# Optimization experiments

Measured on AMD Instinct MI355X. Metric: run time of the kernel, lower is better.

The kernel has to match this reference:

```python
import jax, jax.numpy as jnp
import numpy as np

C, G, NH, NE = 640, 32, 8, 512
B, H, W, P = 8, 32, 32, 77
HD = C // NH
EPS = 1e-5


def _groupnorm(x, g, b):
    # x: (B, C, H, W); normalize over (C//G, H, W) within each of G groups
    bb, cc, hh, ww = x.shape
    xg = x.reshape(bb, G, cc // G, hh, ww)
    mu = xg.mean(axis=(2, 3, 4), keepdims=True)
    var = xg.var(axis=(2, 3, 4), keepdims=True)
    xg = (xg - mu) * jax.lax.rsqrt(var + EPS)
    return xg.reshape(bb, cc, hh, ww) * g[None, :, None, None] + b[None, :, None, None]


def _layernorm(x, g, b):
    mu = x.mean(axis=-1, keepdims=True)
    var = x.var(axis=-1, keepdims=True)
    return (x - mu) * jax.lax.rsqrt(var + EPS) * g + b


def _split_heads(t):
    # (B, S, C) -> (B, NH, S, HD)
    bb, ss, _ = t.shape
    return t.reshape(bb, ss, NH, HD).transpose(0, 2, 1, 3)


def _attn(q, k, v):
    # q,k,v: (B, NH, S, HD) — manual softmax(q k^T / sqrt(d)) v, as in the source
    scores = jnp.einsum('bhqd,bhkd->bhqk', q, k) / (HD ** 0.5)
    probs = jax.nn.softmax(scores, axis=-1)
    out = jnp.einsum('bhqk,bhkd->bhqd', probs, v)
    bb = q.shape[0]
    return out.transpose(0, 2, 1, 3).reshape(bb, q.shape[2], C)


def unet_attention_fwd(x, p, gn_g, gn_b, ci_w, ci_b, ln1_g, ln1_b,
                       qkv_w, qkv_b, saw_w, saw_b, ln2_g, ln2_b,
                       caq_w, caq_b, cak_w, cak_b, cav_w, cav_b, caw_w, caw_b,
                       ln3_g, ln3_b, g1_w, g1_b, g2_w, g2_b, co_w, co_b):
    residue_long = x
    h = _groupnorm(x, gn_g, gn_b)
    # conv_input: 1x1 conv == per-pixel linear; ci_w: (C_in, C_out)
    h = jnp.einsum('bihw,io->bohw', h, ci_w) + ci_b[None, :, None, None]
    bb, cc, hh, ww = h.shape
    h = h.reshape(bb, cc, hh * ww).transpose(0, 2, 1)  # (B, HW, C)

    # self attention
    res = h
    t = _layernorm(h, ln1_g, ln1_b)
    qkv = t @ qkv_w + qkv_b
    q, k, v = jnp.split(qkv, 3, axis=-1)
    t = _attn(_split_heads(q), _split_heads(k), _split_heads(v))
    h = res + (t @ saw_w + saw_b)

    # cross attention (prompt p: (B, 77, NE))
    res = h
    t = _layernorm(h, ln2_g, ln2_b)
    q = t @ caq_w + caq_b
    k = p @ cak_w + cak_b
    v = p @ cav_w + cav_b
    t = _attn(_split_heads(q), _split_heads(k), _split_heads(v))
    h = res + (t @ caw_w + caw_b)

    # GEGLU MLP (exact GELU, matching torch F.gelu default)
    res = h
    t = _layernorm(h, ln3_g, ln3_b)
    proj = t @ g1_w + g1_b  # (B, HW, 8C)
    a, gate = jnp.split(proj, 2, axis=-1)
    t = a * jax.nn.gelu(gate, approximate=False)
    h = res + (t @ g2_w + g2_b)

    h = h.transpose(0, 2, 1).reshape(bb, cc, hh, ww)
    out = jnp.einsum('bihw,io->bohw', h, co_w) + co_b[None, :, None, None]
    return out + residue_long


def setup_inputs() -> dict:
    keys = jax.random.split(jax.random.key(0), 20)
    ki = iter(keys)
    s = 0.02

    def w(shape):
        return jax.random.normal(next(ki), shape, jnp.float32) * s

    return {
        'x': jax.random.normal(next(ki), (B, C, H, W), jnp.float32),
        'p': jax.random.normal(next(ki), (B, P, NE), jnp.float32),
        'gn_g': jnp.ones((C,), jnp.float32), 'gn_b': jnp.zeros((C,), jnp.float32),
        'ci_w': w((C, C)), 'ci_b': jnp.zeros((C,), jnp.float32),
        'ln1_g': jnp.ones((C,), jnp.float32), 'ln1_b': jnp.zeros((C,), jnp.float32),
        'qkv_w': w((C, 3 * C)), 'qkv_b': jnp.zeros((3 * C,), jnp.float32),
        'saw_w': w((C, C)), 'saw_b': jnp.zeros((C,), jnp.float32),
        'ln2_g': jnp.ones((C,), jnp.float32), 'ln2_b': jnp.zeros((C,), jnp.float32),
        'caq_w': w((C, C)), 'caq_b': jnp.zeros((C,), jnp.float32),
        'cak_w': w((NE, C)), 'cak_b': jnp.zeros((C,), jnp.float32),
        'cav_w': w((NE, C)), 'cav_b': jnp.zeros((C,), jnp.float32),
        'caw_w': w((C, C)), 'caw_b': jnp.zeros((C,), jnp.float32),
        'ln3_g': jnp.ones((C,), jnp.float32), 'ln3_b': jnp.zeros((C,), jnp.float32),
        'g1_w': w((C, 8 * C)), 'g1_b': jnp.zeros((8 * C,), jnp.float32),
        'g2_w': w((4 * C, C)), 'g2_b': jnp.zeros((C,), jnp.float32),
        'co_w': w((C, C)), 'co_b': jnp.zeros((C,), jnp.float32),
    }


def reference(x, p, gn_g, gn_b, ci_w, ci_b, ln1_g, ln1_b,
              qkv_w, qkv_b, saw_w, saw_b, ln2_g, ln2_b,
              caq_w, caq_b, cak_w, cak_b, cav_w, cav_b, caw_w, caw_b,
              ln3_g, ln3_b, g1_w, g1_b, g2_w, g2_b, co_w, co_b):
    return unet_attention_fwd(x, p, gn_g, gn_b, ci_w, ci_b, ln1_g, ln1_b,
                              qkv_w, qkv_b, saw_w, saw_b, ln2_g, ln2_b,
                              caq_w, caq_b, cak_w, cak_b, cav_w, cav_b, caw_w, caw_b,
                              ln3_g, ln3_b, g1_w, g1_b, g2_w, g2_b, co_w, co_b)
```

## Files before the change

### kernel.cpp

```cpp
#include <hip/hip_runtime.h>
#include <math.h>

typedef unsigned short u16;
typedef __attribute__((ext_vector_type(8))) short short8;
typedef __attribute__((ext_vector_type(4))) float f32x4;

#define DI static __device__ __forceinline__

DI float bf2f(u16 u) { union { unsigned u; float f; } c; c.u = (unsigned)u << 16; return c.f; }
DI u16 f2bf(float f) {
  union { float f; unsigned u; } c; c.f = f;
  unsigned r = c.u + 0x7fffu + ((c.u >> 16) & 1u);
  return (u16)(r >> 16);
}

DI void gload16(const u16* g, u16* l) {
  __builtin_amdgcn_global_load_lds(
      (const __attribute__((address_space(1))) unsigned int*)g,
      (__attribute__((address_space(3))) unsigned int*)l, 16, 0, 0);
}

DI void xcd_swz(int& bx, int& by, int gx, int gy) {
  int id = by * gx + bx;
  int n = gx * gy;
  int q = n >> 3, r = n & 7;
  int xcd = id & 7, k = id >> 3;
  int s = (xcd < r) ? (xcd * (q + 1) + k) : (r * (q + 1) + (xcd - r) * q + k);
  bx = s % gx;
  by = s / gx;
}

struct PrepDesc { const float* src; u16* dst; int K, N, nbx, boff, perm; };
struct PrepArgs { PrepDesc d[10]; };

__global__ __launch_bounds__(256) void prep_all(PrepArgs a) {
  int bid = blockIdx.x;
  int i = 0;
  while (i < 9 && bid >= a.d[i + 1].boff) i++;
  const PrepDesc D = a.d[i];
  int rel = bid - D.boff;
  int bx = rel % D.nbx, by = rel / D.nbx;
  int K = D.K, N = D.N;
  __shared__ float tile[32][33];
  int k0 = by * 32, n0 = bx * 32;
  int tid = threadIdx.x;
  int ni = tid & 31, ki8 = tid >> 5;
  for (int q = 0; q < 4; q++) {
    int k = ki8 + q * 8;
    tile[k][ni] = D.src[(size_t)(k0 + k) * N + n0 + ni];
  }
  __syncthreads();
  int kj = tid & 31, nj8 = tid >> 5;
  for (int q = 0; q < 4; q++) {
    int n = nj8 + q * 8;
    int nold = n0 + n;
    int rowp = nold;
    if (D.perm) {
      rowp = (nold < 2560) ? ((nold >> 5) * 64 + (nold & 31))
                           : (((nold - 2560) >> 5) * 64 + 32 + (nold & 31));
    }
    D.dst[(size_t)rowp * K + k0 + kj] = f2bf(tile[kj][n]);
  }
}

__global__ __launch_bounds__(256) void conv_bf16(const float* __restrict__ in,
                                                 u16* __restrict__ out, long n) {
  long i = (long)blockIdx.x * 256 + threadIdx.x;
  if (i < n) out[i] = f2bf(in[i]);
}

__global__ __launch_bounds__(256) void concat2(const float* __restrict__ a,
                                               const float* __restrict__ b,
                                               float* __restrict__ o, int n) {
  int i = blockIdx.x * 256 + threadIdx.x;
  if (i < n) o[i] = a[i];
  else if (i < 2 * n) o[i] = b[i - n];
}

__global__ __launch_bounds__(256) void gn_stats(const float* __restrict__ x,
                                                float* __restrict__ mean_o,
                                                float* __restrict__ rstd_o) {
  int bg = blockIdx.x;
  const float4* p = (const float4*)(x + (size_t)bg * 20480);
  float s = 0.f, sq = 0.f;
  for (int i = threadIdx.x; i < 5120; i += 256) {
    float4 v = p[i];
    s += v.x + v.y + v.z + v.w;
    sq += v.x * v.x + v.y * v.y + v.z * v.z + v.w * v.w;
  }
  for (int off = 1; off < 64; off <<= 1) { s += __shfl_xor(s, off); sq += __shfl_xor(sq, off); }
  __shared__ float ps[4], pq[4];
  int w = threadIdx.x >> 6;
  if ((threadIdx.x & 63) == 0) { ps[w] = s; pq[w] = sq; }
  __syncthreads();
  if (threadIdx.x == 0) {
    float S = ps[0] + ps[1] + ps[2] + ps[3];
    float Q = pq[0] + pq[1] + pq[2] + pq[3];
    float mu = S / 20480.f;
    float var = Q / 20480.f - mu * mu;
    mean_o[bg] = mu;
    rstd_o[bg] = rsqrtf(var + 1e-5f);
  }
}

__global__ __launch_bounds__(256) void gn_apply(const float* __restrict__ x,
                                                const float* __restrict__ mean_,
                                                const float* __restrict__ rstd_,
                                                const float* __restrict__ g,
                                                const float* __restrict__ bb,
                                                u16* __restrict__ out) {
  __shared__ float tile[32][33];
  int b = blockIdx.z, c0 = blockIdx.y * 32, s0 = blockIdx.x * 32;
  int tid = threadIdx.x;
  int si = tid & 31, ci8 = tid >> 5;
  for (int i = 0; i < 4; i++) {
    int c = c0 + ci8 + i * 8;
    int gg = c / 20;
    float mu = mean_[b * 32 + gg], rs = rstd_[b * 32 + gg];
    float v = x[((size_t)b * 640 + c) * 1024 + s0 + si];
    tile[ci8 + i * 8][si] = (v - mu) * rs * g[c] + bb[c];
  }
  __syncthreads();
  int cj = tid & 31, sj8 = tid >> 5;
  for (int i = 0; i < 4; i++) {
    int sj = sj8 + i * 8;
    out[((size_t)b * 1024 + s0 + sj) * 640 + c0 + cj] = f2bf(tile[cj][sj]);
  }
}

__global__ __launch_bounds__(256) void ln_kernel(const float* __restrict__ in,
                                                 const float* __restrict__ g,
                                                 const float* __restrict__ bb,
                                                 u16* __restrict__ out) {
  int t = blockIdx.x * 4 + (threadIdx.x >> 6);
  int lane = threadIdx.x & 63;
  const float* row = in + (size_t)t * 640;
  float xv[10], s = 0.f, sq = 0.f;
  for (int j = 0; j < 10; j++) {
    xv[j] = row[lane + j * 64];
    s += xv[j];
    sq += xv[j] * xv[j];
  }
  for (int off = 1; off < 64; off <<= 1) { s += __shfl_xor(s, off); sq += __shfl_xor(sq, off); }
  float mu = s * (1.f / 640.f);
  float var = sq * (1.f / 640.f) - mu * mu;
  float rstd = rsqrtf(var + 1e-5f);
  for (int j = 0; j < 10; j++) {
    int c = lane + j * 64;
    out[(size_t)t * 640 + c] = f2bf((xv[j] - mu) * rstd * g[c] + bb[c]);
  }
}


DI const short8* fragp(const u16* unit, int row, int g4) {
  int off = row * 64 + g4 * 16;
  off ^= ((off >> 7) & 3) << 4;
  return (const short8*)((const char*)unit + off);
}

template <int MODE>
__global__ __launch_bounds__(512, 1) void gemm256(const u16* __restrict__ A,
                                                  const u16* __restrict__ Bt,
                                                  const float* __restrict__ bias,
                                                  void* outp, const float* res,
                                                  int M, int N, int K) {
  __shared__ __align__(16) u16 As[4][8192];
  __shared__ __align__(16) u16 Bs[4][8192];
  const int tid = threadIdx.x;
  const int lane = tid & 63, wid = tid >> 6;
  const int wm = wid >> 2, wn = wid & 3;
  const int rq = lane & 15, g4 = lane >> 4;
  int bx = blockIdx.x, by = blockIdx.y;
  xcd_swz(bx, by, gridDim.x, gridDim.y);
  const int m0 = bx * 256, n0 = by * 256;

  int D0 = tid * 16;
  int so = D0 ^ (((D0 >> 7) & 3) << 4);
  const int srow = so >> 6;
  const int sk16 = (so & 63) >> 1;

  f32x4 acc[8][4] = {};
  const int nt = K >> 5;

#define STG_A(kt)                                                              \
  {                                                                            \
    gload16(A + (size_t)(m0 + srow) * K + (kt)*32 + sk16,                      \
            &As[(kt) & 3][0] + tid * 8);                                       \
    gload16(A + (size_t)(m0 + 128 + srow) * K + (kt)*32 + sk16,                \
            &As[(kt) & 3][4096] + tid * 8);                                    \
  }
#define STG_B(kt)                                                              \
  {                                                                            \
    gload16(Bt + (size_t)(n0 + srow) * K + (kt)*32 + sk16,                     \
            &Bs[(kt) & 3][0] + tid * 8);                                       \
    gload16(Bt + (size_t)(n0 + 128 + srow) * K + (kt)*32 + sk16,               \
            &Bs[(kt) & 3][4096] + tid * 8);                                    \
  }
#define BAR asm volatile("s_barrier" ::: "memory")

#define PH1(T)                                                                 \
  {                                                                            \
    const u16* Au = &As[(T) & 3][0];                                           \
    const u16* Bu = &Bs[(T) & 3][0];                                           \
    _Pragma("unroll") for (int i = 0; i < 4; i++)                              \
        af[i] = *fragp(Au, wm * 128 + i * 16 + rq, g4);                        \
    _Pragma("unroll") for (int j = 0; j < 4; j++)                              \
        bf[j] = *fragp(Bu, wn * 64 + j * 16 + rq, g4);                         \
    BAR;                                                                       \
    asm volatile("s_waitcnt lgkmcnt(0)" ::: "memory");                         \
    __builtin_amdgcn_sched_barrier(0);                                         \
    __builtin_amdgcn_s_setprio(1);                                             \
    _Pragma("unroll") for (int i = 0; i < 4; i++)                              \
        _Pragma("unroll") for (int j = 0; j < 4; j++)                          \
            acc[i][j] =                                                        \
        __builtin_amdgcn_mfma_f32_16x16x32_bf16(af[i], bf[j], acc[i][j], 0, 0, 0); \
    __builtin_amdgcn_s_setprio(0);                                             \
  }

#define PH2(T, DO_STG, WSTR)                                                   \
  {                                                                            \
    const u16* Au = &As[(T) & 3][0];                                           \
    _Pragma("unroll") for (int i = 0; i < 4; i++)                              \
        af[i] = *fragp(Au, wm * 128 + 64 + i * 16 + rq, g4);                   \
    if (DO_STG) { STG_A((T) + 3); STG_B((T) + 3); }                            \
    asm volatile(WSTR ::: "memory");                                           \
    BAR;                                                                       \
    asm volatile("s_waitcnt lgkmcnt(0)" ::: "memory");                         \
    __builtin_amdgcn_sched_barrier(0);                                         \
    __builtin_amdgcn_s_setprio(1);                                             \
    _Pragma("unroll") for (int i = 0; i < 4; i++)                              \
        _Pragma("unroll") for (int j = 0; j < 4; j++)                          \
            acc[4 + i][j] =                                                    \
        __builtin_amdgcn_mfma_f32_16x16x32_bf16(af[i], bf[j], acc[4 + i][j], 0, 0, 0); \
    __builtin_amdgcn_s_setprio(0);                                             \
  }

  STG_A(0); STG_B(0); STG_A(1); STG_B(1); STG_A(2); STG_B(2);
  asm volatile("s_waitcnt vmcnt(8)" ::: "memory");
  BAR;

  short8 af[4], bf[4];
  int t = 0;
  for (; t < nt - 3; t++) {
    PH1(t);
    PH2(t, true, "s_waitcnt vmcnt(8)");
  }
  PH1(t); PH2(t, false, "s_waitcnt vmcnt(4)"); t++;
  PH1(t); PH2(t, false, "s_waitcnt vmcnt(0)"); t++;
  PH1(t); PH2(t, false, "s_nop 0");

  if (MODE == 5) {
#pragma unroll
    for (int mf = 0; mf < 8; mf++) {
      int mb = m0 + wm * 128 + mf * 16 + g4 * 4;
#pragma unroll
      for (int j = 0; j < 2; j++) {
        int n = n0 + wn * 64 + j * 16 + rq;
        int c = (n >> 6) * 32 + (n & 31);
        float ba = bias[c];
        float bg = bias[2560 + c];
#pragma unroll
        for (int r = 0; r < 4; r++) {
          float a = acc[mf][j][r] + ba;
          float gt = acc[mf][j + 2][r] + bg;
          float gl = 0.5f * gt * (1.f + erff(gt * 0.70710678f));
          ((u16*)outp)[(size_t)(mb + r) * 2560 + c] = f2bf(a * gl);
        }
      }
    }
  } else {
#pragma unroll
    for (int mf = 0; mf < 8; mf++) {
#pragma unroll
      for (int j = 0; j < 4; j++) {
        int n = n0 + wn * 64 + j * 16 + rq;
        if (n >= N) continue;
        float bv = bias[n];
        int mb = m0 + wm * 128 + mf * 16 + g4 * 4;
        f32x4 v = acc[mf][j];
#pragma unroll
        for (int r = 0; r < 4; r++) {
          size_t o = (size_t)(mb + r) * N + n;
          ((u16*)outp)[o] = f2bf(v[r] + bv);
        }
      }
    }
  }
  (void)res;
#undef STG_A
#undef STG_B
#undef PH1
#undef PH2
#undef BAR
}

template <int MODE>
__global__ __launch_bounds__(256) void gemm_bt(const u16* __restrict__ A,
                                               const u16* __restrict__ Bt,
                                               const float* __restrict__ bias,
                                               void* outp, const float* res,
                                               int M, int N, int K) {
  __shared__ __align__(16) u16 As[4][128 * 32];
  __shared__ __align__(16) u16 Bs[4][128 * 32];
  const int tid = threadIdx.x;
  const int lane = tid & 63, wid = tid >> 6;
  const int wm = wid >> 1, wn = wid & 1;
  int bx = blockIdx.x, by = blockIdx.y;
  xcd_swz(bx, by, gridDim.x, gridDim.y);
  const int m0 = bx * 128, n0 = by * 128;
  const int rq = lane & 15, g4 = lane >> 4;

  const int srow = tid >> 2;
  const int scol = tid & 3;
  int gmA0 = m0 + srow;        if (gmA0 >= M) gmA0 = M - 1;
  int gmA1 = m0 + 64 + srow;   if (gmA1 >= M) gmA1 = M - 1;
  const u16* gA0 = A + (size_t)gmA0 * K + scol * 8;
  const u16* gA1 = A + (size_t)gmA1 * K + scol * 8;
  const u16* gB0 = Bt + (size_t)(n0 + srow) * K + scol * 8;
  const u16* gB1 = Bt + (size_t)(n0 + 64 + srow) * K + scol * 8;
  u16* lA0 = &As[0][srow * 32 + scol * 8];
  u16* lA1 = &As[0][(64 + srow) * 32 + scol * 8];
  u16* lB0 = &Bs[0][srow * 32 + scol * 8];
  u16* lB1 = &Bs[0][(64 + srow) * 32 + scol * 8];

  f32x4 acc[4][4] = {};

  auto STAGE = [&](int buf, int k0) {
    int o = buf * (128 * 32);
    gload16(gA0 + k0, lA0 + o);
    gload16(gA1 + k0, lA1 + o);
    gload16(gB0 + k0, lB0 + o);
    gload16(gB1 + k0, lB1 + o);
  };
  auto COMPUTE = [&](int buf) {
    short8 af[4], bfr[4];
    for (int i = 0; i < 4; i++)
      af[i] = *(const short8*)&As[buf][(wm * 64 + i * 16 + rq) * 32 + g4 * 8];
    for (int j = 0; j < 4; j++)
      bfr[j] = *(const short8*)&Bs[buf][(wn * 64 + j * 16 + rq) * 32 + g4 * 8];
    __builtin_amdgcn_s_setprio(1);
    for (int i = 0; i < 4; i++)
      for (int j = 0; j < 4; j++)
        acc[i][j] = __builtin_amdgcn_mfma_f32_16x16x32_bf16(af[i], bfr[j], acc[i][j], 0, 0, 0);
    __builtin_amdgcn_s_setprio(0);
  };

  const int nk = K >> 5;
  STAGE(0, 0);
  STAGE(1, 32);
  int t = 0;
  for (; t < nk - 2; t++) {
    STAGE((t + 2) & 3, (t + 2) << 5);
    asm volatile("s_waitcnt vmcnt(8)" ::: "memory");
    __builtin_amdgcn_s_barrier();
    COMPUTE(t & 3);
  }
  asm volatile("s_waitcnt vmcnt(4)" ::: "memory");
  __builtin_amdgcn_s_barrier();
  COMPUTE(t & 3);
  t++;
  asm volatile("s_waitcnt vmcnt(0)" ::: "memory");
  __builtin_amdgcn_s_barrier();
  COMPUTE(t & 3);

  for (int j = 0; j < 4; j++) {
    int n = n0 + wn * 64 + j * 16 + rq;
    float bv = bias[n];
    for (int i = 0; i < 4; i++) {
      int mb = m0 + wm * 64 + i * 16 + g4 * 4;
      f32x4 v = acc[i][j];
      if (MODE == 3) {
        int b = mb >> 10, sp = mb & 1023;
        size_t o = ((size_t)b * 640 + n) * 1024 + sp;
        f32x4 xv = *(const f32x4*)(res + o);
        f32x4 ov;
        for (int r = 0; r < 4; r++) ov[r] = v[r] + bv + xv[r];
        *(f32x4*)((float*)outp + o) = ov;
      } else {
        for (int r = 0; r < 4; r++) {
          int m = mb + r;
          if (m >= M) break;
          size_t o = (size_t)m * N + n;
          float val = v[r] + bv;
          if (MODE == 0)
            ((float*)outp)[o] = val;
          else if (MODE == 1)
            ((u16*)outp)[o] = f2bf(val);
          else if (MODE == 2)
            ((float*)outp)[o] = val + res[o];
          else
            ((u16*)outp)[o] = f2bf(val + res[o]);
        }
      }
    }
  }
}

__global__ __launch_bounds__(256) void attn_kernel(const u16* __restrict__ Qb, int ldq, long qbs,
                                                   const u16* __restrict__ Kb, int ldk, long kbs,
                                                   const u16* __restrict__ Vb,
                                                   u16* __restrict__ Ob, int ldo, long obs,
                                                   int Sk, float scale) {
  __shared__ __align__(16) u16 Ks[64 * 96];
  __shared__ __align__(16) u16 Vt[80 * 64];
  __shared__ __align__(16) u16 Ps[4][16 * 72];
  const short8 zero = {0, 0, 0, 0, 0, 0, 0, 0};
  const int tid = threadIdx.x;
  const int lane = tid & 63, w = tid >> 6;
  const int rq = lane & 15, g4 = lane >> 4;
  const int b = blockIdx.z, h = blockIdx.y;
  const u16* Q = Qb + (size_t)b * qbs + h * 80;
  const u16* Kp = Kb + (size_t)b * kbs + h * 80;
  const u16* Vp = Vb + (size_t)b * kbs + h * 80;
  u16* Op = Ob + (size_t)b * obs + h * 80;
  const int q0 = blockIdx.x * 64 + w * 16;
  const float Af = scale * 1.44269504f;

  short8 qa[3];
#pragma unroll
  for (int kk = 0; kk < 3; kk++) {
    int d = kk * 32 + g4 * 8;
    qa[kk] = (d < 80) ? *(const short8*)(Q + (size_t)(q0 + rq) * ldq + d) : zero;
  }
  f32x4 oacc[5] = {};
  float m_run = -1e30f, l_run = 0.f;

  const int nkt = (Sk + 63) >> 6;
  for (int kt = 0; kt < nkt; kt++) {
    const int kbase = kt * 64;
    for (int s = tid; s < 768; s += 256) {
      int row = s / 12, c = s % 12;
      int kidx = kbase + row;
      short8 v = zero;
      if (c < 10 && kidx < Sk) v = *(const short8*)(Kp + (size_t)kidx * ldk + c * 8);
      int byte = row * 192 + c * 16;
      byte ^= (row & 7) << 4;
      *(short8*)((char*)Ks + byte) = v;
    }
    for (int s = tid; s < 320; s += 256) {
      int k2 = (s & 31) * 2, c = s >> 5;
      int k0i = kbase + k2;
      short8 v0 = zero, v1 = zero;
      if (k0i < Sk) v0 = *(const short8*)(Vp + (size_t)k0i * ldk + c * 8);
      if (k0i + 1 < Sk) v1 = *(const short8*)(Vp + (size_t)(k0i + 1) * ldk + c * 8);
#pragma unroll
      for (int jj = 0; jj < 8; jj++) {
        int d = c * 8 + jj;
        unsigned cm = (unsigned)(u16)v0[jj] | ((unsigned)(u16)v1[jj] << 16);
        int byte = d * 128 + k2 * 2;
        byte ^= (d & 7) << 4;
        *(unsigned*)((char*)Vt + byte) = cm;
      }
    }
    __syncthreads();

    f32x4 sc[4] = {};
#pragma unroll
    for (int n = 0; n < 4; n++)
#pragma unroll
      for (int kk = 0; kk < 3; kk++) {
        int row = n * 16 + rq;
        int byte = row * 192 + (kk * 32 + g4 * 8) * 2;
        byte ^= (rq & 7) << 4;
        short8 kb = *(const short8*)((const char*)Ks + byte);
        sc[n] = __builtin_amdgcn_mfma_f32_16x16x32_bf16(kb, qa[kk], sc[n], 0, 0, 0);
      }
    const bool full = (kbase + 64 <= Sk);
    if (!full) {
#pragma unroll
      for (int n = 0; n < 4; n++)
#pragma unroll
        for (int r = 0; r < 4; r++)
          if (kbase + n * 16 + g4 * 4 + r >= Sk) sc[n][r] = -1e30f;
    }
    float t0 = fmaxf(fmaxf(sc[0][0], sc[0][1]), fmaxf(sc[0][2], sc[0][3]));
    float t1 = fmaxf(fmaxf(sc[1][0], sc[1][1]), fmaxf(sc[1][2], sc[1][3]));
    float t2 = fmaxf(fmaxf(sc[2][0], sc[2][1]), fmaxf(sc[2][2], sc[2][3]));
    float t3 = fmaxf(fmaxf(sc[3][0], sc[3][1]), fmaxf(sc[3][2], sc[3][3]));
    float tm = fmaxf(fmaxf(t0, t1), fmaxf(t2, t3));
    tm = fmaxf(tm, __shfl_xor(tm, 16));
    tm = fmaxf(tm, __shfl_xor(tm, 32));
    if (!__all(tm <= m_run + 48.0f)) {
      float mn = fmaxf(m_run, tm);
      float sf = exp2f(Af * (m_run - mn));
      m_run = mn;
      l_run *= sf;
      float sfo[4];
#pragma unroll
      for (int r = 0; r < 4; r++) sfo[r] = __shfl(sf, g4 * 4 + r);
#pragma unroll
      for (int nn = 0; nn < 5; nn++)
#pragma unroll
        for (int r = 0; r < 4; r++) oacc[nn][r] *= sfo[r];
    }
    const float Am = Af * m_run;
    float rs0 = 0.f, rs1 = 0.f;
#pragma unroll
    for (int n = 0; n < 4; n++) {
      float p0 = exp2f(fmaf(Af, sc[n][0], -Am));
      float p1 = exp2f(fmaf(Af, sc[n][1], -Am));
      float p2 = exp2f(fmaf(Af, sc[n][2], -Am));
      float p3 = exp2f(fmaf(Af, sc[n][3], -Am));
      sc[n][0] = p0; sc[n][1] = p1; sc[n][2] = p2; sc[n][3] = p3;
      rs0 += p0 + p1;
      rs1 += p2 + p3;
    }
    float rsum = rs0 + rs1;
    rsum += __shfl_xor(rsum, 16);
    rsum += __shfl_xor(rsum, 32);
    l_run += rsum;
#pragma unroll
    for (int n = 0; n < 4; n++) {
      unsigned pk0, pk1;
      asm("v_cvt_pk_bf16_f32 %0, %1, %2" : "=v"(pk0) : "v"(sc[n][0]), "v"(sc[n][1]));
      asm("v_cvt_pk_bf16_f32 %0, %1, %2" : "=v"(pk1) : "v"(sc[n][2]), "v"(sc[n][3]));
      int base = rq * 72 + n * 16 + g4 * 4;
      *(unsigned*)&Ps[w][base] = pk0;
      *(unsigned*)&Ps[w][base + 2] = pk1;
    }
    __builtin_amdgcn_s_setprio(1);
#pragma unroll
    for (int s = 0; s < 2; s++) {
      short8 pa = *(const short8*)&Ps[w][rq * 72 + s * 32 + g4 * 8];
#pragma unroll
      for (int nn = 0; nn < 5; nn++) {
        int row = nn * 16 + rq;
        int byte = row * 128 + (s * 32 + g4 * 8) * 2;
        byte ^= (rq & 7) << 4;
        short8 vb = *(const short8*)((const char*)Vt + byte);
        oacc[nn] = __builtin_amdgcn_mfma_f32_16x16x32_bf16(pa, vb, oacc[nn], 0, 0, 0);
      }
    }
    __builtin_amdgcn_s_setprio(0);
    __syncthreads();
  }
  float lo[4];
#pragma unroll
  for (int r = 0; r < 4; r++) lo[r] = 1.0f / __shfl(l_run, g4 * 4 + r);
#pragma unroll
  for (int nn = 0; nn < 5; nn++)
#pragma unroll
    for (int r = 0; r < 4; r++)
      Op[(size_t)(q0 + g4 * 4 + r) * ldo + nn * 16 + rq] = f2bf(oacc[nn][r] * lo[r]);
}

extern "C" void kernel_launch(void* const* d_in, const int* in_sizes, int n_in,
                              void* d_out, int out_size, void* d_ws, size_t ws_size,
                              hipStream_t stream) {
  (void)in_sizes; (void)n_in; (void)out_size; (void)ws_size;
  const float* x = (const float*)d_in[0];
  const float* p = (const float*)d_in[1];
  const float* gn_g = (const float*)d_in[2];
  const float* gn_b = (const float*)d_in[3];
  const float* ci_w = (const float*)d_in[4];
  const float* ci_b = (const float*)d_in[5];
  const float* ln1_g = (const float*)d_in[6];
  const float* ln1_b = (const float*)d_in[7];
  const float* qkv_w = (const float*)d_in[8];
  const float* qkv_b = (const float*)d_in[9];
  const float* saw_w = (const float*)d_in[10];
  const float* saw_b = (const float*)d_in[11];
  const float* ln2_g = (const float*)d_in[12];
  const float* ln2_b = (const float*)d_in[13];
  const float* caq_w = (const float*)d_in[14];
  const float* caq_b = (const float*)d_in[15];
  const float* cak_w = (const float*)d_in[16];
  const float* cak_b = (const float*)d_in[17];
  const float* cav_w = (const float*)d_in[18];
  const float* cav_b = (const float*)d_in[19];
  const float* caw_w = (const float*)d_in[20];
  const float* caw_b = (const float*)d_in[21];
  const float* ln3_g = (const float*)d_in[22];
  const float* ln3_b = (const float*)d_in[23];
  const float* g1_w = (const float*)d_in[24];
  const float* g1_b = (const float*)d_in[25];
  const float* g2_w = (const float*)d_in[26];
  const float* g2_b = (const float*)d_in[27];
  const float* co_w = (const float*)d_in[28];
  const float* co_b = (const float*)d_in[29];
  float* out = (float*)d_out;

  char* ws = (char*)d_ws;
  size_t off = 0;
  auto alloc = [&](size_t bytes) {
    size_t o = off;
    off += (bytes + 255) & ~(size_t)255;
    return o;
  };
  u16* WCI = (u16*)(ws + alloc((size_t)768 * 640 * 2));
  u16* WQKV = (u16*)(ws + alloc((size_t)2048 * 640 * 2));
  u16* WSAW = (u16*)(ws + alloc((size_t)768 * 640 * 2));
  u16* WCAQ = (u16*)(ws + alloc((size_t)768 * 640 * 2));
  u16* WCAKV = (u16*)(ws + alloc((size_t)1280 * 512 * 2));
  u16* WCAW = (u16*)(ws + alloc((size_t)768 * 640 * 2));
  u16* WG1 = (u16*)(ws + alloc((size_t)5120 * 640 * 2));
  u16* WG2 = (u16*)(ws + alloc((size_t)768 * 2560 * 2));
  u16* WCO = (u16*)(ws + alloc((size_t)768 * 640 * 2));
  u16* X = (u16*)(ws + alloc((size_t)8192 * 640 * 2));
  u16* Y = (u16*)(ws + alloc((size_t)8192 * 640 * 2));
  float* F1 = (float*)(ws + alloc((size_t)8192 * 640 * 4));
  u16* QKV = (u16*)(ws + alloc((size_t)8192 * 1920 * 2));
  u16* PBF = (u16*)(ws + alloc((size_t)616 * 512 * 2));
  u16* KVC = (u16*)(ws + alloc((size_t)616 * 1280 * 2));
  u16* TG = (u16*)(ws + alloc((size_t)8192 * 2560 * 2));
  float* GNM = (float*)(ws + alloc(256 * 4));
  float* GNR = (float*)(ws + alloc(256 * 4));
  float* CBIAS = (float*)(ws + alloc(1280 * 4));

  PrepArgs pa;
  int boff = 0;
  auto addw = [&](int idx, const float* src, u16* dst, int K, int N, int perm) {
    pa.d[idx].src = src; pa.d[idx].dst = dst;
    pa.d[idx].K = K; pa.d[idx].N = N;
    pa.d[idx].nbx = N / 32; pa.d[idx].boff = boff; pa.d[idx].perm = perm;
    boff += (N / 32) * (K / 32);
  };
  addw(0, ci_w, WCI, 640, 640, 0);
  addw(1, qkv_w, WQKV, 640, 1920, 0);
  addw(2, saw_w, WSAW, 640, 640, 0);
  addw(3, caq_w, WCAQ, 640, 640, 0);
  addw(4, cak_w, WCAKV, 512, 640, 0);
  addw(5, cav_w, WCAKV + (size_t)640 * 512, 512, 640, 0);
  addw(6, caw_w, WCAW, 640, 640, 0);
  addw(7, g1_w, WG1, 640, 5120, 1);
  addw(8, g2_w, WG2, 2560, 640, 0);
  addw(9, co_w, WCO, 640, 640, 0);
  prep_all<<<boff, 256, 0, stream>>>(pa);
  conv_bf16<<<1232, 256, 0, stream>>>(p, PBF, (long)616 * 512);
  concat2<<<5, 256, 0, stream>>>(cak_b, cav_b, CBIAS, 640);

  gn_stats<<<256, 256, 0, stream>>>(x, GNM, GNR);
  gn_apply<<<dim3(32, 20, 8), 256, 0, stream>>>(x, GNM, GNR, gn_g, gn_b, X);

  const float scale = 0.11180339887498949f;

  gemm_bt<0><<<dim3(64, 5), 256, 0, stream>>>(X, WCI, ci_b, F1, nullptr, 8192, 640, 640);
  ln_kernel<<<2048, 256, 0, stream>>>(F1, ln1_g, ln1_b, Y);
  gemm256<1><<<dim3(32, 8), 512, 0, stream>>>(Y, WQKV, qkv_b, QKV, nullptr, 8192, 1920, 640);
  attn_kernel<<<dim3(16, 8, 8), 256, 0, stream>>>(QKV, 1920, (long)1024 * 1920,
                                                  QKV + 640, 1920, (long)1024 * 1920,
                                                  QKV + 1280, X, 640, (long)1024 * 640,
                                                  1024, scale);
  gemm_bt<2><<<dim3(64, 5), 256, 0, stream>>>(X, WSAW, saw_b, F1, F1, 8192, 640, 640);
  ln_kernel<<<2048, 256, 0, stream>>>(F1, ln2_g, ln2_b, Y);
  gemm_bt<1><<<dim3(64, 5), 256, 0, stream>>>(Y, WCAQ, caq_b, X, nullptr, 8192, 640, 640);
  gemm_bt<1><<<dim3(5, 10), 256, 0, stream>>>(PBF, WCAKV, CBIAS, KVC, nullptr, 616, 1280, 512);
  attn_kernel<<<dim3(16, 8, 8), 256, 0, stream>>>(X, 640, (long)1024 * 640,
                                                  KVC, 1280, (long)77 * 1280,
                                                  KVC + 640, Y, 640, (long)1024 * 640,
                                                  77, scale);
  gemm_bt<2><<<dim3(64, 5), 256, 0, stream>>>(Y, WCAW, caw_b, F1, F1, 8192, 640, 640);
  ln_kernel<<<2048, 256, 0, stream>>>(F1, ln3_g, ln3_b, X);
  gemm256<5><<<dim3(32, 20), 512, 0, stream>>>(X, WG1, g1_b, TG, nullptr, 8192, 5120, 640);
  gemm_bt<4><<<dim3(64, 5), 256, 0, stream>>>(TG, WG2, g2_b, X, F1, 8192, 640, 2560);
  gemm_bt<3><<<dim3(64, 5), 256, 0, stream>>>(X, WCO, co_b, out, x, 8192, 640, 640);
}
```

Measured before the change: 475.2 us.

## Replace 256x256 GEMM with swizzled 128-tile and new 64x128 tile kernels

Removes the 512-thread 256x256 gemm256 kernel and routes the QKV and GEGLU GEMMs through the 128x128 gemm_bt, which gains a fused GEGLU epilogue. Adds a gemm_bt64 kernel with 64x128 tiles for all N=640 GEMMs, doubling the number of workgroups so the 256 CUs are better filled. Also switches gemm_bt's LDS layout to the XOR-swizzled fragment addressing to cut bank conflicts. In exchange, the smaller tiles give less operand reuse per block and use a simpler pipeline than the removed kernel.

New measurement: 486.4 us. 2.3% more time.

```diff
diff --git a/kernel.cpp b/kernel.cpp
--- a/kernel.cpp
+++ b/kernel.cpp
@@ -28,6 +28,12 @@
   int s = (xcd < r) ? (xcd * (q + 1) + k) : (r * (q + 1) + (xcd - r) * q + k);
   bx = s % gx;
   by = s / gx;
+}
+
+DI const short8* fragp(const u16* unit, int row, int g4) {
+  int off = row * 64 + g4 * 16;
+  off ^= ((off >> 7) & 3) << 4;
+  return (const short8*)((const char*)unit + off);
 }
 
 struct PrepDesc { const float* src; u16* dst; int K, N, nbx, boff, perm; };
@@ -151,147 +157,16 @@
   }
 }
 
-
-DI const short8* fragp(const u16* unit, int row, int g4) {
-  int off = row * 64 + g4 * 16;
-  off ^= ((off >> 7) & 3) << 4;
-  return (const short8*)((const char*)unit + off);
-}
-
 template <int MODE>
-__global__ __launch_bounds__(512, 1) void gemm256(const u16* __restrict__ A,
-                                                  const u16* __restrict__ Bt,
-                                                  const float* __restrict__ bias,
-                                                  void* outp, const float* res,
-                                                  int M, int N, int K) {
-  __shared__ __align__(16) u16 As[4][8192];
-  __shared__ __align__(16) u16 Bs[4][8192];
-  const int tid = threadIdx.x;
-  const int lane = tid & 63, wid = tid >> 6;
-  const int wm = wid >> 2, wn = wid & 3;
-  const int rq = lane & 15, g4 = lane >> 4;
-  int bx = blockIdx.x, by = blockIdx.y;
-  xcd_swz(bx, by, gridDim.x, gridDim.y);
-  const int m0 = bx * 256, n0 = by * 256;
-
-  int D0 = tid * 16;
-  int so = D0 ^ (((D0 >> 7) & 3) << 4);
-  const int srow = so >> 6;
-  const int sk16 = (so & 63) >> 1;
-
-  f32x4 acc[8][4] = {};
-  const int nt = K >> 5;
-
-#define STG_A(kt)                                                              \
-  {                                                                            \
-    gload16(A + (size_t)(m0 + srow) * K + (kt)*32 + sk16,                      \
-            &As[(kt) & 3][0] + tid * 8);                                       \
-    gload16(A + (size_t)(m0 + 128 + srow) * K + (kt)*32 + sk16,                \
-            &As[(kt) & 3][4096] + tid * 8);                                    \
-  }
-#define STG_B(kt)                                                              \
-  {                                                                            \
-    gload16(Bt + (size_t)(n0 + srow) * K + (kt)*32 + sk16,                     \
-            &Bs[(kt) & 3][0] + tid * 8);                                       \
-    gload16(Bt + (size_t)(n0 + 128 + srow) * K + (kt)*32 + sk16,               \
-            &Bs[(kt) & 3][4096] + tid * 8);                                    \
-  }
-#define BAR asm volatile("s_barrier" ::: "memory")
-
-#define PH1(T)                                                                 \
-  {                                                                            \
-    const u16* Au = &As[(T) & 3][0];                                           \
-    const u16* Bu = &Bs[(T) & 3][0];                                           \
-    _Pragma("unroll") for (int i = 0; i < 4; i++)                              \
-        af[i] = *fragp(Au, wm * 128 + i * 16 + rq, g4);                        \
-    _Pragma("unroll") for (int j = 0; j < 4; j++)                              \
-        bf[j] = *fragp(Bu, wn * 64 + j * 16 + rq, g4);                         \
-    BAR;                                                                       \
-    asm volatile("s_waitcnt lgkmcnt(0)" ::: "memory");                         \
-    __builtin_amdgcn_sched_barrier(0);                                         \
-    __builtin_amdgcn_s_setprio(1);                                             \
-    _Pragma("unroll") for (int i = 0; i < 4; i++)                              \
-        _Pragma("unroll") for (int j = 0; j < 4; j++)                          \
-            acc[i][j] =                                                        \
-        __builtin_amdgcn_mfma_f32_16x16x32_bf16(af[i], bf[j], acc[i][j], 0, 0, 0); \
-    __builtin_amdgcn_s_setprio(0);                                             \
-  }
-
-#define PH2(T, DO_STG, WSTR)                                                   \
-  {                                                                            \
-    const u16* Au = &As[(T) & 3][0];                                           \
-    _Pragma("unroll") for (int i = 0; i < 4; i++)                              \
-        af[i] = *fragp(Au, wm * 128 + 64 + i * 16 + rq, g4);                   \
-    if (DO_STG) { STG_A((T) + 3); STG_B((T) + 3); }                            \
-    asm volatile(WSTR ::: "memory");                                           \
-    BAR;                                                                       \
-    asm volatile("s_waitcnt lgkmcnt(0)" ::: "memory");                         \
-    __builtin_amdgcn_sched_barrier(0);                                         \
-    __builtin_amdgcn_s_setprio(1);                                             \
-    _Pragma("unroll") for (int i = 0; i < 4; i++)                              \
-        _Pragma("unroll") for (int j = 0; j < 4; j++)                          \
-            acc[4 + i][j] =                                                    \
-        __builtin_amdgcn_mfma_f32_16x16x32_bf16(af[i], bf[j], acc[4 + i][j], 0, 0, 0); \
-    __builtin_amdgcn_s_setprio(0);                                             \
-  }
-
-  STG_A(0); STG_B(0); STG_A(1); STG_B(1); STG_A(2); STG_B(2);
-  asm volatile("s_waitcnt vmcnt(8)" ::: "memory");
-  BAR;
-
-  short8 af[4], bf[4];
-  int t = 0;
-  for (; t < nt - 3; t++) {
-    PH1(t);
-    PH2(t, true, "s_waitcnt vmcnt(8)");
-  }
-  PH1(t); PH2(t, false, "s_waitcnt vmcnt(4)"); t++;
-  PH1(t); PH2(t, false, "s_waitcnt vmcnt(0)"); t++;
-  PH1(t); PH2(t, false, "s_nop 0");
-
-  if (MODE == 5) {
-#pragma unroll
-    for (int mf = 0; mf < 8; mf++) {
-      int mb = m0 + wm * 128 + mf * 16 + g4 * 4;
-#pragma unroll
-      for (int j = 0; j < 2; j++) {
-        int n = n0 + wn * 64 + j * 16 + rq;
-        int c = (n >> 6) * 32 + (n & 31);
-        float ba = bias[c];
-        float bg = bias[2560 + c];
-#pragma unroll
-        for (int r = 0; r < 4; r++) {
-          float a = acc[mf][j][r] + ba;
-          float gt = acc[mf][j + 2][r] + bg;
-          float gl = 0.5f * gt * (1.f + erff(gt * 0.70710678f));
-          ((u16*)outp)[(size_t)(mb + r) * 2560 + c] = f2bf(a * gl);
-        }
-      }
-    }
-  } else {
-#pragma unroll
-    for (int mf = 0; mf < 8; mf++) {
-#pragma unroll
-      for (int j = 0; j < 4; j++) {
-        int n = n0 + wn * 64 + j * 16 + rq;
-        if (n >= N) continue;
-        float bv = bias[n];
-        int mb = m0 + wm * 128 + mf * 16 + g4 * 4;
-        f32x4 v = acc[mf][j];
-#pragma unroll
-        for (int r = 0; r < 4; r++) {
-          size_t o = (size_t)(mb + r) * N + n;
-          ((u16*)outp)[o] = f2bf(v[r] + bv);
-        }
-      }
-    }
-  }
-  (void)res;
-#undef STG_A
-#undef STG_B
-#undef PH1
-#undef PH2
-#undef BAR
+DI void store_elem(void* outp, const float* res, size_t o, float val) {
+  if (MODE == 0)
+    ((float*)outp)[o] = val;
+  else if (MODE == 1)
+    ((u16*)outp)[o] = f2bf(val);
+  else if (MODE == 2)
+    ((float*)outp)[o] = val + res[o];
+  else
+    ((u16*)outp)[o] = f2bf(val + res[o]);
 }
 
 template <int MODE>
@@ -300,8 +175,8 @@
                                                const float* __restrict__ bias,
                                                void* outp, const float* res,
                                                int M, int N, int K) {
-  __shared__ __align__(16) u16 As[4][128 * 32];
-  __shared__ __align__(16) u16 Bs[4][128 * 32];
+  __shared__ __align__(16) u16 As[4][4096];
+  __shared__ __align__(16) u16 Bs[4][4096];
   const int tid = threadIdx.x;
   const int lane = tid & 63, wid = tid >> 6;
   const int wm = wid >> 1, wn = wid & 1;
@@ -310,34 +185,31 @@
   const int m0 = bx * 128, n0 = by * 128;
   const int rq = lane & 15, g4 = lane >> 4;
 
-  const int srow = tid >> 2;
-  const int scol = tid & 3;
-  int gmA0 = m0 + srow;        if (gmA0 >= M) gmA0 = M - 1;
-  int gmA1 = m0 + 64 + srow;   if (gmA1 >= M) gmA1 = M - 1;
-  const u16* gA0 = A + (size_t)gmA0 * K + scol * 8;
-  const u16* gA1 = A + (size_t)gmA1 * K + scol * 8;
-  const u16* gB0 = Bt + (size_t)(n0 + srow) * K + scol * 8;
-  const u16* gB1 = Bt + (size_t)(n0 + 64 + srow) * K + scol * 8;
-  u16* lA0 = &As[0][srow * 32 + scol * 8];
-  u16* lA1 = &As[0][(64 + srow) * 32 + scol * 8];
-  u16* lB0 = &Bs[0][srow * 32 + scol * 8];
-  u16* lB1 = &Bs[0][(64 + srow) * 32 + scol * 8];
+  int D0 = tid * 16;
+  int so = D0 ^ (((D0 >> 7) & 3) << 4);
+  const int srowS = so >> 6;
+  const int sk16 = (so & 63) >> 1;
+  int gmA0 = m0 + srowS;       if (gmA0 >= M) gmA0 = M - 1;
+  int gmA1 = m0 + 64 + srowS;  if (gmA1 >= M) gmA1 = M - 1;
+  const u16* gA0 = A + (size_t)gmA0 * K + sk16;
+  const u16* gA1 = A + (size_t)gmA1 * K + sk16;
+  const u16* gB0 = Bt + (size_t)(n0 + srowS) * K + sk16;
+  const u16* gB1 = Bt + (size_t)(n0 + 64 + srowS) * K + sk16;
 
   f32x4 acc[4][4] = {};
 
   auto STAGE = [&](int buf, int k0) {
-    int o = buf * (128 * 32);
-    gload16(gA0 + k0, lA0 + o);
-    gload16(gA1 + k0, lA1 + o);
-    gload16(gB0 + k0, lB0 + o);
-    gload16(gB1 + k0, lB1 + o);
+    gload16(gA0 + k0, &As[buf][tid * 8]);
+    gload16(gA1 + k0, &As[buf][2048 + tid * 8]);
+    gload16(gB0 + k0, &Bs[buf][tid * 8]);
+    gload16(gB1 + k0, &Bs[buf][2048 + tid * 8]);
   };
   auto COMPUTE = [&](int buf) {
     short8 af[4], bfr[4];
     for (int i = 0; i < 4; i++)
-      af[i] = *(const short8*)&As[buf][(wm * 64 + i * 16 + rq) * 32 + g4 * 8];
+      af[i] = *fragp(&As[buf][0], wm * 64 + i * 16 + rq, g4);
     for (int j = 0; j < 4; j++)
-      bfr[j] = *(const short8*)&Bs[buf][(wn * 64 + j * 16 + rq) * 32 + g4 * 8];
+      bfr[j] = *fragp(&Bs[buf][0], wn * 64 + j * 16 + rq, g4);
     __builtin_amdgcn_s_setprio(1);
     for (int i = 0; i < 4; i++)
       for (int j = 0; j < 4; j++)
@@ -363,6 +235,27 @@
   __builtin_amdgcn_s_barrier();
   COMPUTE(t & 3);
 
+  if (MODE == 5) {
+#pragma unroll
+    for (int i = 0; i < 4; i++) {
+      int mb = m0 + wm * 64 + i * 16 + g4 * 4;
+#pragma unroll
+      for (int j = 0; j < 2; j++) {
+        int n = n0 + wn * 64 + j * 16 + rq;
+        int c = (n >> 6) * 32 + (n & 31);
+        float ba = bias[c];
+        float bg = bias[2560 + c];
+#pragma unroll
+        for (int r = 0; r < 4; r++) {
+          float a = acc[i][j][r] + ba;
+          float gt = acc[i][j + 2][r] + bg;
+          float gl = 0.5f * gt * (1.f + erff(gt * 0.70710678f));
+          ((u16*)outp)[(size_t)(mb + r) * 2560 + c] = f2bf(a * gl);
+        }
+      }
+    }
+    return;
+  }
   for (int j = 0; j < 4; j++) {
     int n = n0 + wn * 64 + j * 16 + rq;
     float bv = bias[n];
@@ -380,16 +273,94 @@
         for (int r = 0; r < 4; r++) {
           int m = mb + r;
           if (m >= M) break;
-          size_t o = (size_t)m * N + n;
-          float val = v[r] + bv;
-          if (MODE == 0)
-            ((float*)outp)[o] = val;
-          else if (MODE == 1)
-            ((u16*)outp)[o] = f2bf(val);
-          else if (MODE == 2)
-            ((float*)outp)[o] = val + res[o];
-          else
-            ((u16*)outp)[o] = f2bf(val + res[o]);
+          store_elem<MODE>(outp, res, (size_t)m * N + n, v[r] + bv);
+        }
+      }
+    }
+  }
+}
+
+template <int MODE>
+__global__ __launch_bounds__(256) void gemm_bt64(const u16* __restrict__ A,
+                                                 const u16* __restrict__ Bt,
+                                                 const float* __restrict__ bias,
+                                                 void* outp, const float* res,
+                                                 int M, int N, int K) {
+  __shared__ __align__(16) u16 As[4][2048];
+  __shared__ __align__(16) u16 Bs[4][4096];
+  const int tid = threadIdx.x;
+  const int lane = tid & 63, wid = tid >> 6;
+  const int wm = wid >> 1, wn = wid & 1;
+  int bx = blockIdx.x, by = blockIdx.y;
+  xcd_swz(bx, by, gridDim.x, gridDim.y);
+  const int m0 = bx * 64, n0 = by * 128;
+  const int rq = lane & 15, g4 = lane >> 4;
+
+  int D0 = tid * 16;
+  int so = D0 ^ (((D0 >> 7) & 3) << 4);
+  const int srowS = so >> 6;
+  const int sk16 = (so & 63) >> 1;
+  int gmA = m0 + srowS;  if (gmA >= M) gmA = M - 1;
+  const u16* gA = A + (size_t)gmA * K + sk16;
+  const u16* gB0 = Bt + (size_t)(n0 + srowS) * K + sk16;
+  const u16* gB1 = Bt + (size_t)(n0 + 64 + srowS) * K + sk16;
+
+  f32x4 acc[2][4] = {};
+
+  auto STAGE = [&](int buf, int k0) {
+    gload16(gA + k0, &As[buf][tid * 8]);
+    gload16(gB0 + k0, &Bs[buf][tid * 8]);
+    gload16(gB1 + k0, &Bs[buf][2048 + tid * 8]);
+  };
+  auto COMPUTE = [&](int buf) {
+    short8 af[2], bfr[4];
+    for (int i = 0; i < 2; i++)
+      af[i] = *fragp(&As[buf][0], wm * 32 + i * 16 + rq, g4);
+    for (int j = 0; j < 4; j++)
+      bfr[j] = *fragp(&Bs[buf][0], wn * 64 + j * 16 + rq, g4);
+    __builtin_amdgcn_s_setprio(1);
+    for (int i = 0; i < 2; i++)
+      for (int j = 0; j < 4; j++)
+        acc[i][j] = __builtin_amdgcn_mfma_f32_16x16x32_bf16(af[i], bfr[j], acc[i][j], 0, 0, 0);
+    __builtin_amdgcn_s_setprio(0);
+  };
+
+  const int nk = K >> 5;
+  STAGE(0, 0);
+  STAGE(1, 32);
+  int t = 0;
+  for (; t < nk - 2; t++) {
+    STAGE((t + 2) & 3, (t + 2) << 5);
+    asm volatile("s_waitcnt vmcnt(6)" ::: "memory");
+    __builtin_amdgcn_s_barrier();
+    COMPUTE(t & 3);
+  }
+  asm volatile("s_waitcnt vmcnt(3)" ::: "memory");
+  __builtin_amdgcn_s_barrier();
+  COMPUTE(t & 3);
+  t++;
+  asm volatile("s_waitcnt vmcnt(0)" ::: "memory");
+  __builtin_amdgcn_s_barrier();
+  COMPUTE(t & 3);
+
+  for (int j = 0; j < 4; j++) {
+    int n = n0 + wn * 64 + j * 16 + rq;
+    float bv = bias[n];
+    for (int i = 0; i < 2; i++) {
+      int mb = m0 + wm * 32 + i * 16 + g4 * 4;
+      f32x4 v = acc[i][j];
+      if (MODE == 3) {
+        int b = mb >> 10, sp = mb & 1023;
+        size_t o = ((size_t)b * 640 + n) * 1024 + sp;
+        f32x4 xv = *(const f32x4*)(res + o);
+        f32x4 ov;
+        for (int r = 0; r < 4; r++) ov[r] = v[r] + bv + xv[r];
+        *(f32x4*)((float*)outp + o) = ov;
+      } else {
+        for (int r = 0; r < 4; r++) {
+          int m = mb + r;
+          if (m >= M) break;
+          store_elem<MODE>(outp, res, (size_t)m * N + n, v[r] + bv);
         }
       }
     }
@@ -634,24 +605,24 @@
 
   const float scale = 0.11180339887498949f;
 
-  gemm_bt<0><<<dim3(64, 5), 256, 0, stream>>>(X, WCI, ci_b, F1, nullptr, 8192, 640, 640);
+  gemm_bt64<0><<<dim3(128, 5), 256, 0, stream>>>(X, WCI, ci_b, F1, nullptr, 8192, 640, 640);
   ln_kernel<<<2048, 256, 0, stream>>>(F1, ln1_g, ln1_b, Y);
-  gemm256<1><<<dim3(32, 8), 512, 0, stream>>>(Y, WQKV, qkv_b, QKV, nullptr, 8192, 1920, 640);
+  gemm_bt<1><<<dim3(64, 15), 256, 0, stream>>>(Y, WQKV, qkv_b, QKV, nullptr, 8192, 1920, 640);
   attn_kernel<<<dim3(16, 8, 8), 256, 0, stream>>>(QKV, 1920, (long)1024 * 1920,
                                                   QKV + 640, 1920, (long)1024 * 1920,
                                                   QKV + 1280, X, 640, (long)1024 * 640,
                                                   1024, scale);
-  gemm_bt<2><<<dim3(64, 5), 256, 0, stream>>>(X, WSAW, saw_b, F1, F1, 8192, 640, 640);
+  gemm_bt64<2><<<dim3(128, 5), 256, 0, stream>>>(X, WSAW, saw_b, F1, F1, 8192, 640, 640);
   ln_kernel<<<2048, 256, 0, stream>>>(F1, ln2_g, ln2_b, Y);
-  gemm_bt<1><<<dim3(64, 5), 256, 0, stream>>>(Y, WCAQ, caq_b, X, nullptr, 8192, 640, 640);
-  gemm_bt<1><<<dim3(5, 10), 256, 0, stream>>>(PBF, WCAKV, CBIAS, KVC, nullptr, 616, 1280, 512);
+  gemm_bt64<1><<<dim3(128, 5), 256, 0, stream>>>(Y, WCAQ, caq_b, X, nullptr, 8192, 640, 640);
+  gemm_bt64<1><<<dim3(10, 10), 256, 0, stream>>>(PBF, WCAKV, CBIAS, KVC, nullptr, 616, 1280, 512);
   attn_kernel<<<dim3(16, 8, 8), 256, 0, stream>>>(X, 640, (long)1024 * 640,
                                                   KVC, 1280, (long)77 * 1280,
                                                   KVC + 640, Y, 640, (long)1024 * 640,
                                                   77, scale);
-  gemm_bt<2><<<dim3(64, 5), 256, 0, stream>>>(Y, WCAW, caw_b, F1, F1, 8192, 640, 640);
+  gemm_bt64<2><<<dim3(128, 5), 256, 0, stream>>>(Y, WCAW, caw_b, F1, F1, 8192, 640, 640);
   ln_kernel<<<2048, 256, 0, stream>>>(F1, ln3_g, ln3_b, X);
-  gemm256<5><<<dim3(32, 20), 512, 0, stream>>>(X, WG1, g1_b, TG, nullptr, 8192, 5120, 640);
-  gemm_bt<4><<<dim3(64, 5), 256, 0, stream>>>(TG, WG2, g2_b, X, F1, 8192, 640, 2560);
-  gemm_bt<3><<<dim3(64, 5), 256, 0, stream>>>(X, WCO, co_b, out, x, 8192, 640, 640);
-}
+  gemm_bt<5><<<dim3(64, 40), 256, 0, stream>>>(X, WG1, g1_b, TG, nullptr, 8192, 5120, 640);
+  gemm_bt64<4><<<dim3(128, 5), 256, 0, stream>>>(TG, WG2, g2_b, X, F1, 8192, 640, 2560);
+  gemm_bt64<3><<<dim3(128, 5), 256, 0, stream>>>(X, WCO, co_b, out, x, 8192, 640, 640);
+}
```

## Shrink N=640 GEMM tiles to 64x128 with swizzled LDS staging

Applied to the files above, without the earlier changes.

Replaces the 128x128 gemm_bt with a 64x128 tile variant and launches twice as many blocks (640 instead of 320) for the 640-wide projections, so all CUs are filled on a 256-CU part. LDS staging now uses an XOR-swizzled layout read through fragp to cut bank conflicts on fragment loads. The trade-off is less operand reuse per block and more redundant B-tile loads.

After: 448.8 us. -5.6%, faster.

```diff
diff --git a/kernel.cpp b/kernel.cpp
--- a/kernel.cpp
+++ b/kernel.cpp
@@ -28,6 +28,12 @@
   int s = (xcd < r) ? (xcd * (q + 1) + k) : (r * (q + 1) + (xcd - r) * q + k);
   bx = s % gx;
   by = s / gx;
+}
+
+DI const short8* fragp(const u16* unit, int row, int g4) {
+  int off = row * 64 + g4 * 16;
+  off ^= ((off >> 7) & 3) << 4;
+  return (const short8*)((const char*)unit + off);
 }
 
 struct PrepDesc { const float* src; u16* dst; int K, N, nbx, boff, perm; };
@@ -151,11 +157,16 @@
   }
 }
 
-
-DI const short8* fragp(const u16* unit, int row, int g4) {
-  int off = row * 64 + g4 * 16;
-  off ^= ((off >> 7) & 3) << 4;
-  return (const short8*)((const char*)unit + off);
+template <int MODE>
+DI void store_elem(void* outp, const float* res, size_t o, float val) {
+  if (MODE == 0)
+    ((float*)outp)[o] = val;
+  else if (MODE == 1)
+    ((u16*)outp)[o] = f2bf(val);
+  else if (MODE == 2)
+    ((float*)outp)[o] = val + res[o];
+  else
+    ((u16*)outp)[o] = f2bf(val + res[o]);
 }
 
 template <int MODE>
@@ -295,51 +306,45 @@
 }
 
 template <int MODE>
-__global__ __launch_bounds__(256) void gemm_bt(const u16* __restrict__ A,
-                                               const u16* __restrict__ Bt,
-                                               const float* __restrict__ bias,
-                                               void* outp, const float* res,
-                                               int M, int N, int K) {
-  __shared__ __align__(16) u16 As[4][128 * 32];
-  __shared__ __align__(16) u16 Bs[4][128 * 32];
+__global__ __launch_bounds__(256) void gemm_bt64(const u16* __restrict__ A,
+                                                 const u16* __restrict__ Bt,
+                                                 const float* __restrict__ bias,
+                                                 void* outp, const float* res,
+                                                 int M, int N, int K) {
+  __shared__ __align__(16) u16 As[4][2048];
+  __shared__ __align__(16) u16 Bs[4][4096];
   const int tid = threadIdx.x;
   const int lane = tid & 63, wid = tid >> 6;
   const int wm = wid >> 1, wn = wid & 1;
   int bx = blockIdx.x, by = blockIdx.y;
   xcd_swz(bx, by, gridDim.x, gridDim.y);
-  const int m0 = bx * 128, n0 = by * 128;
+  const int m0 = bx * 64, n0 = by * 128;
   const int rq = lane & 15, g4 = lane >> 4;
 
-  const int srow = tid >> 2;
-  const int scol = tid & 3;
-  int gmA0 = m0 + srow;        if (gmA0 >= M) gmA0 = M - 1;
-  int gmA1 = m0 + 64 + srow;   if (gmA1 >= M) gmA1 = M - 1;
-  const u16* gA0 = A + (size_t)gmA0 * K + scol * 8;
-  const u16* gA1 = A + (size_t)gmA1 * K + scol * 8;
-  const u16* gB0 = Bt + (size_t)(n0 + srow) * K + scol * 8;
-  const u16* gB1 = Bt + (size_t)(n0 + 64 + srow) * K + scol * 8;
-  u16* lA0 = &As[0][srow * 32 + scol * 8];
-  u16* lA1 = &As[0][(64 + srow) * 32 + scol * 8];
-  u16* lB0 = &Bs[0][srow * 32 + scol * 8];
-  u16* lB1 = &Bs[0][(64 + srow) * 32 + scol * 8];
-
-  f32x4 acc[4][4] = {};
+  int D0 = tid * 16;
+  int so = D0 ^ (((D0 >> 7) & 3) << 4);
+  const int srowS = so >> 6;
+  const int sk16 = (so & 63) >> 1;
+  int gmA = m0 + srowS;  if (gmA >= M) gmA = M - 1;
+  const u16* gA = A + (size_t)gmA * K + sk16;
+  const u16* gB0 = Bt + (size_t)(n0 + srowS) * K + sk16;
+  const u16* gB1 = Bt + (size_t)(n0 + 64 + srowS) * K + sk16;
+
+  f32x4 acc[2][4] = {};
 
   auto STAGE = [&](int buf, int k0) {
-    int o = buf * (128 * 32);
-    gload16(gA0 + k0, lA0 + o);
-    gload16(gA1 + k0, lA1 + o);
-    gload16(gB0 + k0, lB0 + o);
-    gload16(gB1 + k0, lB1 + o);
+    gload16(gA + k0, &As[buf][tid * 8]);
+    gload16(gB0 + k0, &Bs[buf][tid * 8]);
+    gload16(gB1 + k0, &Bs[buf][2048 + tid * 8]);
   };
   auto COMPUTE = [&](int buf) {
-    short8 af[4], bfr[4];
-    for (int i = 0; i < 4; i++)
-      af[i] = *(const short8*)&As[buf][(wm * 64 + i * 16 + rq) * 32 + g4 * 8];
+    short8 af[2], bfr[4];
+    for (int i = 0; i < 2; i++)
+      af[i] = *fragp(&As[buf][0], wm * 32 + i * 16 + rq, g4);
     for (int j = 0; j < 4; j++)
-      bfr[j] = *(const short8*)&Bs[buf][(wn * 64 + j * 16 + rq) * 32 + g4 * 8];
+      bfr[j] = *fragp(&Bs[buf][0], wn * 64 + j * 16 + rq, g4);
     __builtin_amdgcn_s_setprio(1);
-    for (int i = 0; i < 4; i++)
+    for (int i = 0; i < 2; i++)
       for (int j = 0; j < 4; j++)
         acc[i][j] = __builtin_amdgcn_mfma_f32_16x16x32_bf16(af[i], bfr[j], acc[i][j], 0, 0, 0);
     __builtin_amdgcn_s_setprio(0);
@@ -351,11 +356,11 @@
   int t = 0;
   for (; t < nk - 2; t++) {
     STAGE((t + 2) & 3, (t + 2) << 5);
-    asm volatile("s_waitcnt vmcnt(8)" ::: "memory");
+    asm volatile("s_waitcnt vmcnt(6)" ::: "memory");
     __builtin_amdgcn_s_barrier();
     COMPUTE(t & 3);
   }
-  asm volatile("s_waitcnt vmcnt(4)" ::: "memory");
+  asm volatile("s_waitcnt vmcnt(3)" ::: "memory");
   __builtin_amdgcn_s_barrier();
   COMPUTE(t & 3);
   t++;
@@ -366,8 +371,8 @@
   for (int j = 0; j < 4; j++) {
     int n = n0 + wn * 64 + j * 16 + rq;
     float bv = bias[n];
-    for (int i = 0; i < 4; i++) {
-      int mb = m0 + wm * 64 + i * 16 + g4 * 4;
+    for (int i = 0; i < 2; i++) {
+      int mb = m0 + wm * 32 + i * 16 + g4 * 4;
       f32x4 v = acc[i][j];
       if (MODE == 3) {
         int b = mb >> 10, sp = mb & 1023;
@@ -380,16 +385,7 @@
         for (int r = 0; r < 4; r++) {
           int m = mb + r;
           if (m >= M) break;
-          size_t o = (size_t)m * N + n;
-          float val = v[r] + bv;
-          if (MODE == 0)
-            ((float*)outp)[o] = val;
-          else if (MODE == 1)
-            ((u16*)outp)[o] = f2bf(val);
-          else if (MODE == 2)
-            ((float*)outp)[o] = val + res[o];
-          else
-            ((u16*)outp)[o] = f2bf(val + res[o]);
+          store_elem<MODE>(outp, res, (size_t)m * N + n, v[r] + bv);
         }
       }
     }
@@ -634,24 +630,24 @@
 
   const float scale = 0.11180339887498949f;
 
-  gemm_bt<0><<<dim3(64, 5), 256, 0, stream>>>(X, WCI, ci_b, F1, nullptr, 8192, 640, 640);
+  gemm_bt64<0><<<dim3(128, 5), 256, 0, stream>>>(X, WCI, ci_b, F1, nullptr, 8192, 640, 640);
   ln_kernel<<<2048, 256, 0, stream>>>(F1, ln1_g, ln1_b, Y);
   gemm256<1><<<dim3(32, 8), 512, 0, stream>>>(Y, WQKV, qkv_b, QKV, nullptr, 8192, 1920, 640);
   attn_kernel<<<dim3(16, 8, 8), 256, 0, stream>>>(QKV, 1920, (long)1024 * 1920,
                                                   QKV + 640, 1920, (long)1024 * 1920,
                                                   QKV + 1280, X, 640, (long)1024 * 640,
                                                   1024, scale);
-  gemm_bt<2><<<dim3(64, 5), 256, 0, stream>>>(X, WSAW, saw_b, F1, F1, 8192, 640, 640);
+  gemm_bt64<2><<<dim3(128, 5), 256, 0, stream>>>(X, WSAW, saw_b, F1, F1, 8192, 640, 640);
   ln_kernel<<<2048, 256, 0, stream>>>(F1, ln2_g, ln2_b, Y);
-  gemm_bt<1><<<dim3(64, 5), 256, 0, stream>>>(Y, WCAQ, caq_b, X, nullptr, 8192, 640, 640);
-  gemm_bt<1><<<dim3(5, 10), 256, 0, stream>>>(PBF, WCAKV, CBIAS, KVC, nullptr, 616, 1280, 512);
+  gemm_bt64<1><<<dim3(128, 5), 256, 0, stream>>>(Y, WCAQ, caq_b, X, nullptr, 8192, 640, 640);
+  gemm_bt64<1><<<dim3(10, 10), 256, 0, stream>>>(PBF, WCAKV, CBIAS, KVC, nullptr, 616, 1280, 512);
   attn_kernel<<<dim3(16, 8, 8), 256, 0, stream>>>(X, 640, (long)1024 * 640,
                                                   KVC, 1280, (long)77 * 1280,
                                                   KVC + 640, Y, 640, (long)1024 * 640,
                                                   77, scale);
-  gemm_bt<2><<<dim3(64, 5), 256, 0, stream>>>(Y, WCAW, caw_b, F1, F1, 8192, 640, 640);
+  gemm_bt64<2><<<dim3(128, 5), 256, 0, stream>>>(Y, WCAW, caw_b, F1, F1, 8192, 640, 640);
   ln_kernel<<<2048, 256, 0, stream>>>(F1, ln3_g, ln3_b, X);
   gemm256<5><<<dim3(32, 20), 512, 0, stream>>>(X, WG1, g1_b, TG, nullptr, 8192, 5120, 640);
-  gemm_bt<4><<<dim3(64, 5), 256, 0, stream>>>(TG, WG2, g2_b, X, F1, 8192, 640, 2560);
-  gemm_bt<3><<<dim3(64, 5), 256, 0, stream>>>(X, WCO, co_b, out, x, 8192, 640, 640);
-}
+  gemm_bt64<4><<<dim3(128, 5), 256, 0, stream>>>(TG, WG2, g2_b, X, F1, 8192, 640, 2560);
+  gemm_bt64<3><<<dim3(128, 5), 256, 0, stream>>>(X, WCO, co_b, out, x, 8192, 640, 640);
+}
```
